# Performance work log

Hardware: AMD Instinct MI355X
Metric: run time of the kernel (lower is better)

## Reference

```python
import jax, jax.numpy as jnp
import numpy as np


def setup_inputs() -> dict:
    key = jax.random.key(0)
    k1, k2, k3, k4, k5 = jax.random.split(key, 5)
    B, S, D, U = 64, 2048, 512, 512
    he = lambda k, shape: jax.random.normal(k, shape, dtype=jnp.float32) * jnp.sqrt(2.0 / shape[0])
    return {
        "query": jax.random.normal(k1, (B, D), dtype=jnp.float32),
        "values": jax.random.normal(k2, (B, S, D), dtype=jnp.float32),
        "W1": he(k3, (D, U)),
        "W2": he(k4, (D, U)),
        "V1": he(k5, (U, 1)),
    }


def reference(query, values, W1, W2, V1):
    # query: (B, D), values: (B, S, D)
    Q = query @ W1                       # (B, U)
    V = jnp.einsum("bsd,du->bsu", values, W2)  # (B, S, U)
    add = jnp.tanh(Q[:, None, :] + V)    # (B, S, U)
    score = jnp.einsum("bsu,uo->bso", add, V1)  # (B, S, 1)
    attn = jax.nn.softmax(score, axis=1)         # (B, S, 1)
    context = jnp.sum(attn * values, axis=1)     # (B, D)
    return context
```

## Files before the change

### kernel.cpp

```cpp
#include <hip/hip_runtime.h>


typedef __attribute__((ext_vector_type(8))) short bf16x8;
typedef __attribute__((ext_vector_type(4))) float f32x4;

#if __has_builtin(__builtin_amdgcn_exp2f)
__device__ __forceinline__ float fast_exp2(float x) { return __builtin_amdgcn_exp2f(x); }
#else
__device__ __forceinline__ float fast_exp2(float x) { return exp2f(x); }
#endif
#if __has_builtin(__builtin_amdgcn_rcpf)
__device__ __forceinline__ float fast_rcp(float x) { return __builtin_amdgcn_rcpf(x); }
#else
__device__ __forceinline__ float fast_rcp(float x) { return 1.0f / x; }
#endif

__device__ __forceinline__ unsigned short f2bf(float f) {
  unsigned int u = __float_as_uint(f);
  u += 0x7fffu + ((u >> 16) & 1u);
  return (unsigned short)(u >> 16);
}

__global__ void qk(const float* __restrict__ query, const float* __restrict__ W1,
                   float* __restrict__ Q) {
  __shared__ float qrow[512];
  const int b = blockIdx.x, half = blockIdx.y, t = threadIdx.x;
  qrow[t] = query[b * 512 + t];
  qrow[t + 256] = query[b * 512 + t + 256];
  __syncthreads();
  const int u = half * 256 + t;
  float acc = 0.f;
#pragma unroll 8
  for (int k = 0; k < 512; ++k) acc += qrow[k] * W1[(size_t)k * 512 + u];
  Q[b * 512 + u] = acc;
}

__global__ void wt_k(const float* __restrict__ W2, unsigned short* __restrict__ Wtf,
                     float* __restrict__ out0) {
  const int gid = blockIdx.x * 256 + threadIdx.x;
  out0[gid] = 0.f;
  const int lane = gid & 63;
  const int g = gid >> 6;
  const int ks = g & 15, ntile = g >> 4;
  const int l15 = lane & 15, quad = lane >> 4;
  const int n = ntile * 16 + l15;
  const int k0 = ks * 32 + quad * 8;
  unsigned int p[4];
#pragma unroll
  for (int jj = 0; jj < 4; ++jj) {
    const float a = W2[(size_t)(k0 + 2 * jj) * 512 + n];
    const float b = W2[(size_t)(k0 + 2 * jj + 1) * 512 + n];
    p[jj] = (unsigned int)f2bf(a) | ((unsigned int)f2bf(b) << 16);
  }
  *(uint4*)&Wtf[(size_t)gid * 8] = make_uint4(p[0], p[1], p[2], p[3]);
}

__global__ __launch_bounds__(512, 4) void scores_k(
    const float* __restrict__ values, const unsigned short* __restrict__ Wtf,
    const float* __restrict__ Q, const float* __restrict__ V1,
    float* __restrict__ scores) {
  __shared__ __align__(16) unsigned short Ab[64 * 512];
  __shared__ float sAcc[64];

  const int t = threadIdx.x;
  const int lane = t & 63;
  const int w = t >> 6;
  const int quad = lane >> 4;
  const int l15 = lane & 15;
  const int m0 = blockIdx.x * 64;
  const int b = m0 >> 11;

  if (t < 64) sAcc[t] = 0.0f;

  const float* Ag = values + (size_t)m0 * 512;
#pragma unroll
  for (int i = 0; i < 8; ++i) {
    const int c = i * 512 + t;
    const int m = c >> 6;
    const int kc = c & 63;
    const float4* src = (const float4*)(Ag + (size_t)m * 512 + kc * 8);
    const float4 x = src[0], y = src[1];
    const unsigned int p0 = (unsigned int)f2bf(x.x) | ((unsigned int)f2bf(x.y) << 16);
    const unsigned int p1 = (unsigned int)f2bf(x.z) | ((unsigned int)f2bf(x.w) << 16);
    const unsigned int p2 = (unsigned int)f2bf(y.x) | ((unsigned int)f2bf(y.y) << 16);
    const unsigned int p3 = (unsigned int)f2bf(y.z) | ((unsigned int)f2bf(y.w) << 16);
    *(uint4*)&Ab[m * 512 + ((kc ^ (m & 7)) * 8)] = make_uint4(p0, p1, p2, p3);
  }
  __syncthreads();

  f32x4 acc[4][4];
#pragma unroll
  for (int mt = 0; mt < 4; ++mt)
#pragma unroll
    for (int nt = 0; nt < 4; ++nt) acc[mt][nt] = (f32x4){0.f, 0.f, 0.f, 0.f};

  const unsigned short* Bg = Wtf + (size_t)lane * 8;
  const int sw = l15 & 7;

#pragma unroll
  for (int ks = 0; ks < 16; ++ks) {
    bf16x8 bfr[4], af[4];
#pragma unroll
    for (int nt = 0; nt < 4; ++nt)
      bfr[nt] = *(const bf16x8*)(Bg + (size_t)((w * 4 + nt) * 16 + ks) * 512);
#pragma unroll
    for (int mt = 0; mt < 4; ++mt) {
      const int m = mt * 16 + l15;
      af[mt] = *(const bf16x8*)&Ab[m * 512 + (((ks * 4 + quad) ^ sw) * 8)];
    }
#pragma unroll
    for (int mt = 0; mt < 4; ++mt)
#pragma unroll
      for (int nt = 0; nt < 4; ++nt)
        acc[mt][nt] = __builtin_amdgcn_mfma_f32_16x16x32_bf16(af[mt], bfr[nt],
                                                              acc[mt][nt], 0, 0, 0);
  }

  float part[4][4];
#pragma unroll
  for (int mt = 0; mt < 4; ++mt)
#pragma unroll
    for (int r = 0; r < 4; ++r) part[mt][r] = 0.f;

#pragma unroll
  for (int nt = 0; nt < 4; ++nt) {
    const int n = w * 64 + nt * 16 + l15;
    const float qv = Q[b * 512 + n];
    const float v1 = V1[n];
#pragma unroll
    for (int mt = 0; mt < 4; ++mt)
#pragma unroll
      for (int r = 0; r < 4; ++r) {
        const float x = acc[mt][nt][r] + qv;
        const float e = fast_exp2(x * 2.8853900817779268f);
        const float th = 1.0f - 2.0f * fast_rcp(e + 1.0f);
        part[mt][r] += th * v1;
      }
  }
#pragma unroll
  for (int mt = 0; mt < 4; ++mt)
#pragma unroll
    for (int r = 0; r < 4; ++r) {
      float v = part[mt][r];
      v += __shfl_xor(v, 1);
      v += __shfl_xor(v, 2);
      v += __shfl_xor(v, 4);
      v += __shfl_xor(v, 8);
      if (l15 == 0) atomicAdd(&sAcc[mt * 16 + quad * 4 + r], v);
    }
  __syncthreads();
  if (t < 64) scores[m0 + t] = sAcc[t];
}

__global__ __launch_bounds__(512) void ctx_k(const float* __restrict__ values,
                                             const float* __restrict__ scores,
                                             float* __restrict__ out) {
  __shared__ float red[16];
  __shared__ float wsc[256];
  const int bid = blockIdx.x;
  const int b = bid >> 3, sc = bid & 7;
  const int t = threadIdx.x;
  const float* sb = scores + (size_t)b * 2048;
  const float v0 = sb[t], v1 = sb[t + 512], v2 = sb[t + 1024], v3 = sb[t + 1536];
  float mx = fmaxf(fmaxf(v0, v1), fmaxf(v2, v3));
#pragma unroll
  for (int o = 1; o < 64; o <<= 1) mx = fmaxf(mx, __shfl_xor(mx, o));
  if ((t & 63) == 0) red[t >> 6] = mx;
  __syncthreads();
  mx = fmaxf(fmaxf(fmaxf(red[0], red[1]), fmaxf(red[2], red[3])),
             fmaxf(fmaxf(red[4], red[5]), fmaxf(red[6], red[7])));
  const float L2E = 1.4426950408889634f;
  float sum = fast_exp2((v0 - mx) * L2E) + fast_exp2((v1 - mx) * L2E) +
              fast_exp2((v2 - mx) * L2E) + fast_exp2((v3 - mx) * L2E);
#pragma unroll
  for (int o = 1; o < 64; o <<= 1) sum += __shfl_xor(sum, o);
  if ((t & 63) == 0) red[8 + (t >> 6)] = sum;
  __syncthreads();
  sum = (red[8] + red[9]) + (red[10] + red[11]) + (red[12] + red[13]) +
        (red[14] + red[15]);
  const float inv = 1.0f / sum;
  if (t < 256) wsc[t] = fast_exp2((sb[sc * 256 + t] - mx) * L2E) * inv;
  __syncthreads();
  const float* vb = values + ((size_t)b * 2048 + sc * 256) * 512;
  float acc = 0.f;
#pragma unroll 8
  for (int s = 0; s < 256; ++s) acc += wsc[s] * vb[(size_t)s * 512 + t];
  atomicAdd(&out[b * 512 + t], acc);
}

extern "C" void kernel_launch(void* const* d_in, const int* in_sizes, int n_in,
                              void* d_out, int out_size, void* d_ws, size_t ws_size,
                              hipStream_t stream) {
  const float* query = (const float*)d_in[0];
  const float* values = (const float*)d_in[1];
  const float* W1 = (const float*)d_in[2];
  const float* W2 = (const float*)d_in[3];
  const float* V1 = (const float*)d_in[4];
  float* out = (float*)d_out;

  char* ws = (char*)d_ws;
  float* Qp = (float*)ws;
  unsigned short* Wtp = (unsigned short*)(ws + 131072);
  float* Sp = (float*)(ws + 131072 + 524288);

  qk<<<dim3(64, 2), 256, 0, stream>>>(query, W1, Qp);
  wt_k<<<128, 256, 0, stream>>>(W2, Wtp, out);
  scores_k<<<2048, 512, 0, stream>>>(values, Wtp, Qp, V1, Sp);
  ctx_k<<<512, 512, 0, stream>>>(values, Sp, out);
}
```

Baseline: 498.9 us.

## Switch scores GEMM to 32x32x16 MFMA with rotating B-fragment prefetch

Replaces the 16x16x32 bf16 MFMA tiling in the scores kernel with 32x32x16 MFMA tiles (2x2 per wave). The W2 pre-layout kernel is rewritten to match the new fragment layout. B fragments are software-pipelined through a 4-deep register ring, and each wave starts at a different k-slice offset to spread LDS bank and L2 access. The aim is fewer MFMA issues and LDS A-fragment reads per FLOP and hidden global-load latency for B, with the epilogue reduction adjusted to the 32x32 output layout. The cost is higher register pressure from the 16-wide accumulators plus the prefetch ring.

Result: no change. 501.0 us (+0.4%).

```diff
diff --git a/kernel.cpp b/kernel.cpp
--- a/kernel.cpp
+++ b/kernel.cpp
@@ -2,7 +2,7 @@
 
 
 typedef __attribute__((ext_vector_type(8))) short bf16x8;
-typedef __attribute__((ext_vector_type(4))) float f32x4;
+typedef __attribute__((ext_vector_type(16))) float f32x16;
 
 #if __has_builtin(__builtin_amdgcn_exp2f)
 __device__ __forceinline__ float fast_exp2(float x) { return __builtin_amdgcn_exp2f(x); }
@@ -40,11 +40,10 @@
   const int gid = blockIdx.x * 256 + threadIdx.x;
   out0[gid] = 0.f;
   const int lane = gid & 63;
-  const int g = gid >> 6;
-  const int ks = g & 15, ntile = g >> 4;
-  const int l15 = lane & 15, quad = lane >> 4;
-  const int n = ntile * 16 + l15;
-  const int k0 = ks * 32 + quad * 8;
+  const int frag = gid >> 6;
+  const int ks = frag & 31, nt32 = frag >> 5;
+  const int n = nt32 * 32 + (lane & 31);
+  const int k0 = ks * 16 + (lane >> 5) * 8;
   unsigned int p[4];
 #pragma unroll
   for (int jj = 0; jj < 4; ++jj) {
@@ -65,8 +64,8 @@
   const int t = threadIdx.x;
   const int lane = t & 63;
   const int w = t >> 6;
-  const int quad = lane >> 4;
-  const int l15 = lane & 15;
+  const int hi = lane >> 5;
+  const int l31 = lane & 31;
   const int m0 = blockIdx.x * 64;
   const int b = m0 >> 11;
 
@@ -88,66 +87,86 @@
   }
   __syncthreads();
 
-  f32x4 acc[4][4];
-#pragma unroll
-  for (int mt = 0; mt < 4; ++mt)
-#pragma unroll
-    for (int nt = 0; nt < 4; ++nt) acc[mt][nt] = (f32x4){0.f, 0.f, 0.f, 0.f};
-
-  const unsigned short* Bg = Wtf + (size_t)lane * 8;
-  const int sw = l15 & 7;
-
-#pragma unroll
-  for (int ks = 0; ks < 16; ++ks) {
-    bf16x8 bfr[4], af[4];
-#pragma unroll
-    for (int nt = 0; nt < 4; ++nt)
-      bfr[nt] = *(const bf16x8*)(Bg + (size_t)((w * 4 + nt) * 16 + ks) * 512);
-#pragma unroll
-    for (int mt = 0; mt < 4; ++mt) {
-      const int m = mt * 16 + l15;
-      af[mt] = *(const bf16x8*)&Ab[m * 512 + (((ks * 4 + quad) ^ sw) * 8)];
-    }
-#pragma unroll
-    for (int mt = 0; mt < 4; ++mt)
-#pragma unroll
-      for (int nt = 0; nt < 4; ++nt)
-        acc[mt][nt] = __builtin_amdgcn_mfma_f32_16x16x32_bf16(af[mt], bfr[nt],
+  f32x16 acc[2][2];
+#pragma unroll
+  for (int mt = 0; mt < 2; ++mt)
+#pragma unroll
+    for (int nt = 0; nt < 2; ++nt)
+#pragma unroll
+      for (int r = 0; r < 16; ++r) acc[mt][nt][r] = 0.f;
+
+  const int w4 = w * 4;
+  const unsigned short* Bg0 = Wtf + (size_t)(w * 2) * 32 * 512 + (size_t)lane * 8;
+  const unsigned short* Bg1 = Bg0 + 32 * 512;
+  const int sw = l31 & 7;
+
+  bf16x8 Bb[4][2];
+#pragma unroll
+  for (int p = 0; p < 4; ++p) {
+    const int ksx = (p + w4) & 31;
+    Bb[p][0] = *(const bf16x8*)(Bg0 + (size_t)ksx * 512);
+    Bb[p][1] = *(const bf16x8*)(Bg1 + (size_t)ksx * 512);
+  }
+
+#pragma unroll
+  for (int ks = 0; ks < 32; ++ks) {
+    const int pb = ks & 3;
+    const int ksx = (ks + w4) & 31;
+    const int kc = ksx * 2 + hi;
+    bf16x8 af[2];
+#pragma unroll
+    for (int mt = 0; mt < 2; ++mt) {
+      const int m = mt * 32 + l31;
+      af[mt] = *(const bf16x8*)&Ab[m * 512 + ((kc ^ sw) * 8)];
+    }
+#pragma unroll
+    for (int mt = 0; mt < 2; ++mt)
+#pragma unroll
+      for (int nt = 0; nt < 2; ++nt)
+        acc[mt][nt] = __builtin_amdgcn_mfma_f32_32x32x16_bf16(af[mt], Bb[pb][nt],
                                                               acc[mt][nt], 0, 0, 0);
-  }
-
-  float part[4][4];
-#pragma unroll
-  for (int mt = 0; mt < 4; ++mt)
-#pragma unroll
-    for (int r = 0; r < 4; ++r) part[mt][r] = 0.f;
-
-#pragma unroll
-  for (int nt = 0; nt < 4; ++nt) {
-    const int n = w * 64 + nt * 16 + l15;
-    const float qv = Q[b * 512 + n];
-    const float v1 = V1[n];
-#pragma unroll
-    for (int mt = 0; mt < 4; ++mt)
-#pragma unroll
-      for (int r = 0; r < 4; ++r) {
-        const float x = acc[mt][nt][r] + qv;
+    if (ks < 28) {
+      const int ksn = ((ks + 4) + w4) & 31;
+      Bb[pb][0] = *(const bf16x8*)(Bg0 + (size_t)ksn * 512);
+      Bb[pb][1] = *(const bf16x8*)(Bg1 + (size_t)ksn * 512);
+    }
+  }
+
+  float qv[2], v1v[2];
+#pragma unroll
+  for (int nt = 0; nt < 2; ++nt) {
+    const int n = w * 64 + nt * 32 + l31;
+    qv[nt] = Q[b * 512 + n];
+    v1v[nt] = V1[n];
+  }
+#pragma unroll
+  for (int mt = 0; mt < 2; ++mt) {
+    float rsum[16];
+#pragma unroll
+    for (int reg = 0; reg < 16; ++reg) {
+      float s = 0.f;
+#pragma unroll
+      for (int nt = 0; nt < 2; ++nt) {
+        const float x = acc[mt][nt][reg] + qv[nt];
         const float e = fast_exp2(x * 2.8853900817779268f);
         const float th = 1.0f - 2.0f * fast_rcp(e + 1.0f);
-        part[mt][r] += th * v1;
+        s += th * v1v[nt];
       }
-  }
-#pragma unroll
-  for (int mt = 0; mt < 4; ++mt)
-#pragma unroll
-    for (int r = 0; r < 4; ++r) {
-      float v = part[mt][r];
-      v += __shfl_xor(v, 1);
-      v += __shfl_xor(v, 2);
-      v += __shfl_xor(v, 4);
-      v += __shfl_xor(v, 8);
-      if (l15 == 0) atomicAdd(&sAcc[mt * 16 + quad * 4 + r], v);
-    }
+      s += __shfl_xor(s, 1);
+      s += __shfl_xor(s, 2);
+      s += __shfl_xor(s, 4);
+      s += __shfl_xor(s, 8);
+      s += __shfl_xor(s, 16);
+      rsum[reg] = s;
+    }
+    if (l31 == 0) {
+#pragma unroll
+      for (int reg = 0; reg < 16; ++reg) {
+        const int row = mt * 32 + (reg & 3) + 8 * (reg >> 2) + 4 * hi;
+        atomicAdd(&sAcc[row], rsum[reg]);
+      }
+    }
+  }
   __syncthreads();
   if (t < 64) scores[m0 + t] = sAcc[t];
 }
```
